# Kernel tuning notes

Measured on AMD Instinct MI355X. Metric: run time of the kernel, lower is better.

Reference implementation:

```python
import jax, jax.numpy as jnp
import numpy as np

B, S, D, H = 2, 2048, 1024, 16
HD = D // H


def setup_inputs() -> dict:
    key = jax.random.key(0)
    ks = jax.random.split(key, 16)
    sc = 0.02
    return {
        "hidden_states": jax.random.normal(ks[0], (B, S, D), jnp.float32),
        "Wq": jax.random.normal(ks[1], (D, D), jnp.float32) * sc,
        "bq": jnp.zeros((D,), jnp.float32),
        "Wk": jax.random.normal(ks[2], (D, D), jnp.float32) * sc,
        "bk": jnp.zeros((D,), jnp.float32),
        "Wv": jax.random.normal(ks[3], (D, D), jnp.float32) * sc,
        "bv": jnp.zeros((D,), jnp.float32),
        "Wo": jax.random.normal(ks[4], (D, D), jnp.float32) * sc,
        "bo": jnp.zeros((D,), jnp.float32),
        "rel_W": jax.random.normal(ks[5], (3, 2 * D), jnp.float32) * sc,
        "rel_b": jnp.zeros((3,), jnp.float32),
        "logical_bias": jax.random.normal(ks[6], (H, 3), jnp.float32) * sc,
        "gate_W": jax.random.normal(ks[7], (H, D), jnp.float32) * sc,
        "gate_b": jnp.zeros((H,), jnp.float32),
    }


def reference(hidden_states, Wq, bq, Wk, bk, Wv, bv, Wo, bo,
              rel_W, rel_b, logical_bias, gate_W, gate_b):
    x = hidden_states
    b, s, d = x.shape
    h = gate_W.shape[0]
    hd = d // h
    scale = hd ** 0.5

    q = (x @ Wq.T + bq).reshape(b, s, h, hd)
    k = (x @ Wk.T + bk).reshape(b, s, h, hd)
    v = (x @ Wv.T + bv).reshape(b, s, h, hd)

    # [b, h, i, j] raw attention scores
    attn_scores = jnp.einsum('bihd,bjhd->bhij', q, k) / scale

    # Pairwise relation logits WITHOUT materializing the [b,s,s,2d] concat:
    # cat([h_i, h_j]) @ W.T == h_i @ W[:, :d].T + h_j @ W[:, d:].T
    li = x @ rel_W[:, :d].T   # (b, s, 3) contribution from position i
    lj = x @ rel_W[:, d:].T   # (b, s, 3) contribution from position j
    logits = li[:, :, None, :] + lj[:, None, :, :] + rel_b  # (b, s, s, 3)
    relation_probs = jax.nn.softmax(logits, axis=-1)

    bias = jnp.einsum('bijk,hk->bhij', relation_probs, logical_bias)

    gate = jax.nn.sigmoid(x @ gate_W.T + gate_b)        # (b, s, h)
    gate = jnp.transpose(gate, (0, 2, 1))[..., None]    # (b, h, s, 1)

    attn_scores = attn_scores + gate * bias
    attn_weights = jax.nn.softmax(attn_scores, axis=-1)

    out = jnp.einsum('bhij,bjhd->bihd', attn_weights, v).reshape(b, s, d)
    return out @ Wo.T + bo
```

## Files before the change

### kernel.cpp

```cpp
#include <hip/hip_runtime.h>
#include <math.h>

#define B_   2
#define S_   2048
#define D_   1024
#define H_   16
#define NROW (B_ * S_)

typedef __bf16 bf16_t;
typedef __bf16 bf16x8 __attribute__((ext_vector_type(8)));
typedef __bf16 bf16x4v __attribute__((ext_vector_type(4)));
typedef float  f32x4  __attribute__((ext_vector_type(4)));

#define MFMA16(a, b, c) __builtin_amdgcn_mfma_f32_16x16x32_bf16((a), (b), (c), 0, 0, 0)

__device__ __forceinline__ void glds16(const void* src, void* lds) {
    __builtin_amdgcn_global_load_lds(
        (const __attribute__((address_space(1))) void*)src,
        (__attribute__((address_space(3))) void*)lds, 16, 0, 0);
}

__global__ __launch_bounds__(256)
void cvt_all(const float* __restrict__ x, const float* __restrict__ wq,
             const float* __restrict__ wk, const float* __restrict__ wv,
             const float* __restrict__ wo, bf16_t* __restrict__ xb,
             bf16_t* __restrict__ wqb, bf16_t* __restrict__ wkb,
             bf16_t* __restrict__ wvb, bf16_t* __restrict__ wob) {
    int bid = blockIdx.x;
    const float* src;
    bf16_t* dst;
    int base;
    if (bid < 4096) { src = x; dst = xb; base = bid; }
    else {
        int k = (bid - 4096) >> 10;
        base = (bid - 4096) & 1023;
        src = (k == 0) ? wq : (k == 1) ? wk : (k == 2) ? wv : wo;
        dst = (k == 0) ? wqb : (k == 1) ? wkb : (k == 2) ? wvb : wob;
    }
    int idx = base * 1024 + threadIdx.x * 4;
    float4 v = *(const float4*)&src[idx];
    bf16x4v o;
    o[0] = (bf16_t)v.x; o[1] = (bf16_t)v.y; o[2] = (bf16_t)v.z; o[3] = (bf16_t)v.w;
    *(bf16x4v*)&dst[idx] = o;
}

__global__ __launch_bounds__(256)
void proj_small(const float* __restrict__ x, const float* __restrict__ relW,
                const float* __restrict__ relB, const float* __restrict__ gateW,
                const float* __restrict__ gateB,
                float* __restrict__ EA4, float* __restrict__ EB4,
                float* __restrict__ GA) {
    const int wave = threadIdx.x >> 6;
    const int lane = threadIdx.x & 63;
    const int row  = blockIdx.x * 4 + wave;

    const float* xr = x + (size_t)row * D_;
    float xv[16];
    #pragma unroll
    for (int t = 0; t < 16; ++t) xv[t] = xr[lane + 64 * t];

    for (int c = 0; c < 22; ++c) {
        const float* w;
        if (c < 3)       w = relW + c * (2 * D_);
        else if (c < 6)  w = relW + (c - 3) * (2 * D_) + D_;
        else             w = gateW + (size_t)(c - 6) * D_;
        float s = 0.f;
        #pragma unroll
        for (int t = 0; t < 16; ++t) s += xv[t] * w[lane + 64 * t];
        #pragma unroll
        for (int off = 32; off; off >>= 1) s += __shfl_xor(s, off);
        if (lane == 0) {
            if (c < 3)      EA4[row * 4 + c] = expf(s + relB[c]);
            else if (c < 6) EB4[row * 4 + (c - 3)] = expf(s);
            else            GA[row * H_ + (c - 6)] =
                                1.f / (1.f + expf(-(s + gateB[c - 6])));
        }
    }
}

template<int OUTBF16>
__global__ __launch_bounds__(256)
void gemm_bf16(const bf16_t* __restrict__ A, const bf16_t* __restrict__ W,
               const float* __restrict__ bias, void* __restrict__ Cout,
               int N, int K, float scale) {
    __shared__ __align__(16) bf16_t As[128 * 32];
    __shared__ __align__(16) bf16_t Bs[128 * 32];

    const int tid = threadIdx.x, w = tid >> 6, l = tid & 63;
    const int row0 = blockIdx.y * 128, col0 = blockIdx.x * 128;
    const int wr = w >> 1, wc = w & 1;
    const int p16 = l & 15, g4 = l >> 4;

    f32x4 acc[4][4];
    #pragma unroll
    for (int i = 0; i < 4; ++i)
        #pragma unroll
        for (int j = 0; j < 4; ++j) acc[i][j] = (f32x4){0.f, 0.f, 0.f, 0.f};

    const int r0 = l >> 2, ch = l & 3;
    const int r1 = 16 + r0;
    const int ca0 = (ch ^ ((r0 >> 1) & 3)) << 3;
    const int ca1 = (ch ^ ((r1 >> 1) & 3)) << 3;
    const bf16_t* aS = A + (size_t)(row0 + w * 32) * K;
    const bf16_t* bS = W + (size_t)(col0 + w * 32) * K;
    bf16_t* aD = As + w * 1024;
    bf16_t* bD = Bs + w * 1024;

    for (int k0 = 0; k0 < K; k0 += 32) {
        glds16(aS + (size_t)r0 * K + k0 + ca0, aD);
        glds16(aS + (size_t)r1 * K + k0 + ca1, aD + 512);
        glds16(bS + (size_t)r0 * K + k0 + ca0, bD);
        glds16(bS + (size_t)r1 * K + k0 + ca1, bD + 512);
        __syncthreads();

        bf16x8 af[4], bfr[4];
        #pragma unroll
        for (int mi = 0; mi < 4; ++mi) {
            int row = wr * 64 + mi * 16 + p16;
            int chk = g4 ^ ((row >> 1) & 3);
            af[mi] = *(const bf16x8*)&As[row * 32 + chk * 8];
        }
        #pragma unroll
        for (int nj = 0; nj < 4; ++nj) {
            int row = wc * 64 + nj * 16 + p16;
            int chk = g4 ^ ((row >> 1) & 3);
            bfr[nj] = *(const bf16x8*)&Bs[row * 32 + chk * 8];
        }
        #pragma unroll
        for (int mi = 0; mi < 4; ++mi)
            #pragma unroll
            for (int nj = 0; nj < 4; ++nj)
                acc[mi][nj] = MFMA16(af[mi], bfr[nj], acc[mi][nj]);
        __syncthreads();
    }

    const int cj = col0 + wc * 64 + p16;
    #pragma unroll
    for (int nj = 0; nj < 4; ++nj) {
        int j = cj + nj * 16;
        float bj = bias[j];
        #pragma unroll
        for (int mi = 0; mi < 4; ++mi) {
            int ib = row0 + wr * 64 + mi * 16 + g4 * 4;
            #pragma unroll
            for (int r = 0; r < 4; ++r) {
                float v = (acc[mi][nj][r] + bj) * scale;
                if (OUTBF16)
                    ((bf16_t*)Cout)[(size_t)(ib + r) * N + j] = (bf16_t)v;
                else
                    ((float*)Cout)[(size_t)(ib + r) * N + j] = v;
            }
        }
    }
}

__global__ __launch_bounds__(256)
void flash_mfma(const bf16_t* __restrict__ Q, const bf16_t* __restrict__ Kg,
                const bf16_t* __restrict__ Vg, const float4* __restrict__ EA4,
                const float4* __restrict__ EB4, const float* __restrict__ GA,
                const float* __restrict__ LB, bf16_t* __restrict__ AO) {
    __shared__ __align__(16) bf16_t Ks[64 * 64];
    __shared__ __align__(16) bf16_t Vt[64 * 64];
    __shared__ __align__(16) bf16_t Ps[4][16 * 64];
    __shared__ __align__(16) float  ebs[64 * 4];

    const int tid = threadIdx.x, w = tid >> 6, l = tid & 63;
    const int b = blockIdx.y >> 4, h = blockIdx.y & 15;
    const int i0 = blockIdx.x * 64;
    const size_t rowb = (size_t)b * S_ + i0;
    const int p16 = l & 15, g4 = l >> 4;

    const float lb0 = LB[h * 3 + 0], lb1 = LB[h * 3 + 1], lb2 = LB[h * 3 + 2];

    bf16x8 qf[2];
    {
        const bf16_t* qp = Q + (rowb + w * 16 + p16) * D_ + h * 64 + g4 * 8;
        qf[0] = *(const bf16x8*)qp;
        qf[1] = *(const bf16x8*)(qp + 32);
    }

    float eaR[4][3], cnR[4][3];
    float lsum[4] = {0.f, 0.f, 0.f, 0.f};
    #pragma unroll
    for (int r = 0; r < 4; ++r) {
        size_t gi = rowb + w * 16 + g4 * 4 + r;
        float4 e = EA4[gi];
        float g = GA[gi * H_ + h];
        eaR[r][0] = e.x; eaR[r][1] = e.y; eaR[r][2] = e.z;
        cnR[r][0] = g * e.x * lb0; cnR[r][1] = g * e.y * lb1; cnR[r][2] = g * e.z * lb2;
    }

    f32x4 o[4];
    #pragma unroll
    for (int nb = 0; nb < 4; ++nb) o[nb] = (f32x4){0.f, 0.f, 0.f, 0.f};

    const int vj = tid >> 2, vc = (tid & 3) * 16;
    const int kr0 = l >> 3, kc0 = l & 7;

    for (int j0 = 0; j0 < S_; j0 += 64) {
        const size_t jb = (size_t)b * S_ + j0;
        {
            int rowA = w * 16 + kr0;
            int rowB = rowA + 8;
            glds16(Kg + (jb + rowA) * D_ + h * 64 + ((kc0 ^ (rowA & 7)) << 3),
                   Ks + w * 1024);
            glds16(Kg + (jb + rowB) * D_ + h * 64 + ((kc0 ^ (rowB & 7)) << 3),
                   Ks + w * 1024 + 512);
        }
        bf16x8 v0, v1;
        {
            const bf16_t* vp = Vg + (jb + vj) * D_ + h * 64 + vc;
            v0 = *(const bf16x8*)vp;
            v1 = *(const bf16x8*)(vp + 8);
        }
        if (tid < 64) *(float4*)&ebs[tid * 4] = EB4[jb + tid];
        #pragma unroll
        for (int u = 0; u < 8; ++u) {
            int hd = vc + u;
            int sw = ((hd & 7) ^ ((hd >> 3) & 7)) << 3;
            Vt[hd * 64 + (vj ^ sw)] = v0[u];
        }
        #pragma unroll
        for (int u = 0; u < 8; ++u) {
            int hd = vc + 8 + u;
            int sw = ((hd & 7) ^ ((hd >> 3) & 7)) << 3;
            Vt[hd * 64 + (vj ^ sw)] = v1[u];
        }
        __syncthreads();

        f32x4 s[4];
        #pragma unroll
        for (int nb = 0; nb < 4; ++nb) {
            s[nb] = (f32x4){0.f, 0.f, 0.f, 0.f};
            int row = nb * 16 + p16;
            int sw = row & 7;
            bf16x8 k0v = *(const bf16x8*)&Ks[row * 64 + ((g4    ) ^ sw) * 8];
            bf16x8 k1v = *(const bf16x8*)&Ks[row * 64 + ((g4 + 4) ^ sw) * 8];
            s[nb] = MFMA16(qf[0], k0v, s[nb]);
            s[nb] = MFMA16(qf[1], k1v, s[nb]);
        }

        #pragma unroll
        for (int nb = 0; nb < 4; ++nb) {
            float4 eb = *(const float4*)&ebs[(nb * 16 + p16) * 4];
            #pragma unroll
            for (int r = 0; r < 4; ++r) {
                float Nv = cnR[r][0] * eb.x + cnR[r][1] * eb.y + cnR[r][2] * eb.z;
                float Dv = eaR[r][0] * eb.x + eaR[r][1] * eb.y + eaR[r][2] * eb.z;
                float sv = s[nb][r] + Nv * __builtin_amdgcn_rcpf(Dv);
                float p = __expf(sv);
                bf16_t pb = (bf16_t)p;
                lsum[r] += (float)pb;
                int irow = g4 * 4 + r;
                int jcol = nb * 16 + p16;
                Ps[w][irow * 64 + (jcol ^ ((irow & 7) << 3))] = pb;
            }
        }

        bf16x8 pf0, pf1;
        {
            int sw = p16 & 7;
            pf0 = *(const bf16x8*)&Ps[w][p16 * 64 + ((g4    ) ^ sw) * 8];
            pf1 = *(const bf16x8*)&Ps[w][p16 * 64 + ((g4 + 4) ^ sw) * 8];
        }
        #pragma unroll
        for (int nb = 0; nb < 4; ++nb) {
            int vrow = nb * 16 + p16;
            int sw = (vrow & 7) ^ ((vrow >> 3) & 7);
            bf16x8 vf0 = *(const bf16x8*)&Vt[vrow * 64 + ((g4    ) ^ sw) * 8];
            bf16x8 vf1 = *(const bf16x8*)&Vt[vrow * 64 + ((g4 + 4) ^ sw) * 8];
            o[nb] = MFMA16(pf0, vf0, o[nb]);
            o[nb] = MFMA16(pf1, vf1, o[nb]);
        }
        __syncthreads();
    }

    #pragma unroll
    for (int r = 0; r < 4; ++r) {
        float t = lsum[r];
        t += __shfl_xor(t, 1); t += __shfl_xor(t, 2);
        t += __shfl_xor(t, 4); t += __shfl_xor(t, 8);
        lsum[r] = 1.f / t;
    }
    #pragma unroll
    for (int nb = 0; nb < 4; ++nb)
        #pragma unroll
        for (int r = 0; r < 4; ++r) {
            size_t gi = rowb + w * 16 + g4 * 4 + r;
            AO[gi * D_ + h * 64 + nb * 16 + p16] = (bf16_t)(o[nb][r] * lsum[r]);
        }
}

extern "C" void kernel_launch(void* const* d_in, const int* in_sizes, int n_in,
                              void* d_out, int out_size, void* d_ws, size_t ws_size,
                              hipStream_t stream) {
    const float* x    = (const float*)d_in[0];
    const float* Wq   = (const float*)d_in[1];
    const float* bq   = (const float*)d_in[2];
    const float* Wk   = (const float*)d_in[3];
    const float* bk   = (const float*)d_in[4];
    const float* Wv   = (const float*)d_in[5];
    const float* bv   = (const float*)d_in[6];
    const float* Wo   = (const float*)d_in[7];
    const float* bo   = (const float*)d_in[8];
    const float* relW = (const float*)d_in[9];
    const float* relB = (const float*)d_in[10];
    const float* lb   = (const float*)d_in[11];
    const float* gW   = (const float*)d_in[12];
    const float* gb   = (const float*)d_in[13];

    uint8_t* W8 = (uint8_t*)d_ws;
    bf16_t* xb  = (bf16_t*)(W8);
    bf16_t* wqb = (bf16_t*)(W8 + (8u  << 20));
    bf16_t* wkb = (bf16_t*)(W8 + (10u << 20));
    bf16_t* wvb = (bf16_t*)(W8 + (12u << 20));
    bf16_t* wob = (bf16_t*)(W8 + (14u << 20));
    bf16_t* Qb  = (bf16_t*)(W8 + (16u << 20));
    bf16_t* Kb  = (bf16_t*)(W8 + (24u << 20));
    bf16_t* Vb  = (bf16_t*)(W8 + (32u << 20));
    bf16_t* AOb = (bf16_t*)(W8 + (40u << 20));
    float*  EA  = (float*)(W8 + (48u << 20));
    float*  EB  = (float*)(W8 + (48u << 20) + NROW * 16);
    float*  GAp = (float*)(W8 + (48u << 20) + NROW * 32);

    cvt_all<<<8192, 256, 0, stream>>>(x, Wq, Wk, Wv, Wo, xb, wqb, wkb, wvb, wob);
    proj_small<<<NROW / 4, 256, 0, stream>>>(x, relW, relB, gW, gb, EA, EB, GAp);

    dim3 gg(D_ / 128, NROW / 128);
    gemm_bf16<1><<<gg, 256, 0, stream>>>(xb, wqb, bq, Qb, D_, D_, 0.125f);
    gemm_bf16<1><<<gg, 256, 0, stream>>>(xb, wkb, bk, Kb, D_, D_, 1.f);
    gemm_bf16<1><<<gg, 256, 0, stream>>>(xb, wvb, bv, Vb, D_, D_, 1.f);

    flash_mfma<<<dim3(S_ / 64, B_ * H_), 256, 0, stream>>>(
        Qb, Kb, Vb, (const float4*)EA, (const float4*)EB, GAp, lb, AOb);

    gemm_bf16<0><<<gg, 256, 0, stream>>>(AOb, wob, bo, d_out, D_, D_, 1.f);
}
```

Before: 335.1 us.

## Fuse QKV GEMMs, widen K tile, compute relation bias via MFMA with exp2

```diff
diff --git a/kernel.cpp b/kernel.cpp
--- a/kernel.cpp
+++ b/kernel.cpp
@@ -6,6 +6,7 @@
 #define D_   1024
 #define H_   16
 #define NROW (B_ * S_)
+#define L2E_ 1.4426950408889634f
 
 typedef __bf16 bf16_t;
 typedef __bf16 bf16x8 __attribute__((ext_vector_type(8)));
@@ -13,6 +14,12 @@
 typedef float  f32x4  __attribute__((ext_vector_type(4)));
 
 #define MFMA16(a, b, c) __builtin_amdgcn_mfma_f32_16x16x32_bf16((a), (b), (c), 0, 0, 0)
+
+#if __has_builtin(__builtin_amdgcn_exp2f)
+#define EXP2F(x) __builtin_amdgcn_exp2f(x)
+#else
+#define EXP2F(x) exp2f(x)
+#endif
 
 __device__ __forceinline__ void glds16(const void* src, void* lds) {
     __builtin_amdgcn_global_load_lds(
@@ -78,18 +85,13 @@
     }
 }
 
-template<int OUTBF16>
-__global__ __launch_bounds__(256)
-void gemm_bf16(const bf16_t* __restrict__ A, const bf16_t* __restrict__ W,
-               const float* __restrict__ bias, void* __restrict__ Cout,
-               int N, int K, float scale) {
-    __shared__ __align__(16) bf16_t As[128 * 32];
-    __shared__ __align__(16) bf16_t Bs[128 * 32];
-
+__device__ __forceinline__ void gemm_body128(
+    const bf16_t* __restrict__ A, const bf16_t* __restrict__ W,
+    const float* __restrict__ bias, float scale, int row0, int col0,
+    bf16_t* As, bf16_t* Bs, int outbf16, void* Cout, int N, int K)
+{
     const int tid = threadIdx.x, w = tid >> 6, l = tid & 63;
-    const int row0 = blockIdx.y * 128, col0 = blockIdx.x * 128;
-    const int wr = w >> 1, wc = w & 1;
-    const int p16 = l & 15, g4 = l >> 4;
+    const int wr = w >> 1, wc = w & 1, p16 = l & 15, g4 = l >> 4;
 
     f32x4 acc[4][4];
     #pragma unroll
@@ -97,40 +99,38 @@
         #pragma unroll
         for (int j = 0; j < 4; ++j) acc[i][j] = (f32x4){0.f, 0.f, 0.f, 0.f};
 
-    const int r0 = l >> 2, ch = l & 3;
-    const int r1 = 16 + r0;
-    const int ca0 = (ch ^ ((r0 >> 1) & 3)) << 3;
-    const int ca1 = (ch ^ ((r1 >> 1) & 3)) << 3;
+    const int sr = l >> 3, sc = l & 7;
     const bf16_t* aS = A + (size_t)(row0 + w * 32) * K;
     const bf16_t* bS = W + (size_t)(col0 + w * 32) * K;
-    bf16_t* aD = As + w * 1024;
-    bf16_t* bD = Bs + w * 1024;
-
-    for (int k0 = 0; k0 < K; k0 += 32) {
-        glds16(aS + (size_t)r0 * K + k0 + ca0, aD);
-        glds16(aS + (size_t)r1 * K + k0 + ca1, aD + 512);
-        glds16(bS + (size_t)r0 * K + k0 + ca0, bD);
-        glds16(bS + (size_t)r1 * K + k0 + ca1, bD + 512);
+
+    for (int k0 = 0; k0 < K; k0 += 64) {
+        #pragma unroll
+        for (int i = 0; i < 4; ++i) {
+            int r = i * 8 + sr;
+            int co = k0 + ((sc ^ sr) << 3);
+            glds16(aS + (size_t)r * K + co, As + (w * 32 + i * 8) * 64);
+            glds16(bS + (size_t)r * K + co, Bs + (w * 32 + i * 8) * 64);
+        }
         __syncthreads();
-
-        bf16x8 af[4], bfr[4];
-        #pragma unroll
-        for (int mi = 0; mi < 4; ++mi) {
-            int row = wr * 64 + mi * 16 + p16;
-            int chk = g4 ^ ((row >> 1) & 3);
-            af[mi] = *(const bf16x8*)&As[row * 32 + chk * 8];
-        }
-        #pragma unroll
-        for (int nj = 0; nj < 4; ++nj) {
-            int row = wc * 64 + nj * 16 + p16;
-            int chk = g4 ^ ((row >> 1) & 3);
-            bfr[nj] = *(const bf16x8*)&Bs[row * 32 + chk * 8];
-        }
-        #pragma unroll
-        for (int mi = 0; mi < 4; ++mi)
-            #pragma unroll
-            for (int nj = 0; nj < 4; ++nj)
-                acc[mi][nj] = MFMA16(af[mi], bfr[nj], acc[mi][nj]);
+        #pragma unroll
+        for (int c = 0; c < 2; ++c) {
+            bf16x8 af[4], bfr[4];
+            #pragma unroll
+            for (int mi = 0; mi < 4; ++mi) {
+                int row = wr * 64 + mi * 16 + p16;
+                af[mi] = *(const bf16x8*)&As[row * 64 + (((c * 4 + g4) ^ (row & 7)) << 3)];
+            }
+            #pragma unroll
+            for (int nj = 0; nj < 4; ++nj) {
+                int row = wc * 64 + nj * 16 + p16;
+                bfr[nj] = *(const bf16x8*)&Bs[row * 64 + (((c * 4 + g4) ^ (row & 7)) << 3)];
+            }
+            #pragma unroll
+            for (int mi = 0; mi < 4; ++mi)
+                #pragma unroll
+                for (int nj = 0; nj < 4; ++nj)
+                    acc[mi][nj] = MFMA16(af[mi], bfr[nj], acc[mi][nj]);
+        }
         __syncthreads();
     }
 
@@ -145,13 +145,42 @@
             #pragma unroll
             for (int r = 0; r < 4; ++r) {
                 float v = (acc[mi][nj][r] + bj) * scale;
-                if (OUTBF16)
+                if (outbf16)
                     ((bf16_t*)Cout)[(size_t)(ib + r) * N + j] = (bf16_t)v;
                 else
                     ((float*)Cout)[(size_t)(ib + r) * N + j] = v;
             }
         }
     }
+}
+
+__global__ __launch_bounds__(256)
+void gemm_qkv(const bf16_t* __restrict__ xb,
+              const bf16_t* __restrict__ wq, const bf16_t* __restrict__ wk,
+              const bf16_t* __restrict__ wv,
+              const float* __restrict__ bq, const float* __restrict__ bk,
+              const float* __restrict__ bv,
+              bf16_t* __restrict__ Qb, bf16_t* __restrict__ Kb,
+              bf16_t* __restrict__ Vb) {
+    __shared__ __align__(16) bf16_t As[128 * 64];
+    __shared__ __align__(16) bf16_t Bs[128 * 64];
+    const int seg = blockIdx.x >> 3;
+    const int col0 = (blockIdx.x & 7) * 128;
+    const int row0 = blockIdx.y * 128;
+    const bf16_t* W = (seg == 0) ? wq : (seg == 1) ? wk : wv;
+    const float* bias = (seg == 0) ? bq : (seg == 1) ? bk : bv;
+    bf16_t* C = (seg == 0) ? Qb : (seg == 1) ? Kb : Vb;
+    const float scale = (seg == 0) ? 0.125f * L2E_ : 1.0f;
+    gemm_body128(xb, W, bias, scale, row0, col0, As, Bs, 1, C, D_, D_);
+}
+
+__global__ __launch_bounds__(256)
+void gemm_out(const bf16_t* __restrict__ A, const bf16_t* __restrict__ wo,
+              const float* __restrict__ bo, float* __restrict__ out) {
+    __shared__ __align__(16) bf16_t As[128 * 64];
+    __shared__ __align__(16) bf16_t Bs[128 * 64];
+    gemm_body128(A, wo, bo, 1.0f, blockIdx.y * 128, blockIdx.x * 128,
+                 As, Bs, 0, out, D_, D_);
 }
 
 __global__ __launch_bounds__(256)
@@ -179,17 +208,25 @@
         qf[1] = *(const bf16x8*)(qp + 32);
     }
 
-    float eaR[4][3], cnR[4][3];
+    bf16x8 zer;
+    #pragma unroll
+    for (int u = 0; u < 8; ++u) zer[u] = (bf16_t)0.f;
+    bf16x8 cnf = zer, eaf = zer;
+    {
+        size_t gi = rowb + w * 16 + p16;
+        float4 e = EA4[gi];
+        float g = GA[gi * H_ + h] * L2E_;
+        if (g4 == 0) {
+            cnf[0] = (bf16_t)(g * e.x * lb0);
+            cnf[1] = (bf16_t)(g * e.y * lb1);
+            cnf[2] = (bf16_t)(g * e.z * lb2);
+            eaf[0] = (bf16_t)e.x;
+            eaf[1] = (bf16_t)e.y;
+            eaf[2] = (bf16_t)e.z;
+        }
+    }
+
     float lsum[4] = {0.f, 0.f, 0.f, 0.f};
-    #pragma unroll
-    for (int r = 0; r < 4; ++r) {
-        size_t gi = rowb + w * 16 + g4 * 4 + r;
-        float4 e = EA4[gi];
-        float g = GA[gi * H_ + h];
-        eaR[r][0] = e.x; eaR[r][1] = e.y; eaR[r][2] = e.z;
-        cnR[r][0] = g * e.x * lb0; cnR[r][1] = g * e.y * lb1; cnR[r][2] = g * e.z * lb2;
-    }
-
     f32x4 o[4];
     #pragma unroll
     for (int nb = 0; nb < 4; ++nb) o[nb] = (f32x4){0.f, 0.f, 0.f, 0.f};
@@ -228,6 +265,19 @@
         }
         __syncthreads();
 
+        f32x4 nacc[4], dacc[4];
+        #pragma unroll
+        for (int nb = 0; nb < 4; ++nb) {
+            float4 e = *(const float4*)&ebs[(nb * 16 + p16) * 4];
+            bf16x8 ebf = zer;
+            if (g4 == 0) {
+                ebf[0] = (bf16_t)e.x; ebf[1] = (bf16_t)e.y; ebf[2] = (bf16_t)e.z;
+            }
+            f32x4 z4 = (f32x4){0.f, 0.f, 0.f, 0.f};
+            nacc[nb] = MFMA16(cnf, ebf, z4);
+            dacc[nb] = MFMA16(eaf, ebf, z4);
+        }
+
         f32x4 s[4];
         #pragma unroll
         for (int nb = 0; nb < 4; ++nb) {
@@ -242,13 +292,10 @@
 
         #pragma unroll
         for (int nb = 0; nb < 4; ++nb) {
-            float4 eb = *(const float4*)&ebs[(nb * 16 + p16) * 4];
             #pragma unroll
             for (int r = 0; r < 4; ++r) {
-                float Nv = cnR[r][0] * eb.x + cnR[r][1] * eb.y + cnR[r][2] * eb.z;
-                float Dv = eaR[r][0] * eb.x + eaR[r][1] * eb.y + eaR[r][2] * eb.z;
-                float sv = s[nb][r] + Nv * __builtin_amdgcn_rcpf(Dv);
-                float p = __expf(sv);
+                float sv = s[nb][r] + nacc[nb][r] * __builtin_amdgcn_rcpf(dacc[nb][r]);
+                float p = EXP2F(sv);
                 bf16_t pb = (bf16_t)p;
                 lsum[r] += (float)pb;
                 int irow = g4 * 4 + r;
@@ -326,13 +373,11 @@
     cvt_all<<<8192, 256, 0, stream>>>(x, Wq, Wk, Wv, Wo, xb, wqb, wkb, wvb, wob);
     proj_small<<<NROW / 4, 256, 0, stream>>>(x, relW, relB, gW, gb, EA, EB, GAp);
 
-    dim3 gg(D_ / 128, NROW / 128);
-    gemm_bf16<1><<<gg, 256, 0, stream>>>(xb, wqb, bq, Qb, D_, D_, 0.125f);
-    gemm_bf16<1><<<gg, 256, 0, stream>>>(xb, wkb, bk, Kb, D_, D_, 1.f);
-    gemm_bf16<1><<<gg, 256, 0, stream>>>(xb, wvb, bv, Vb, D_, D_, 1.f);
+    gemm_qkv<<<dim3(24, 32), 256, 0, stream>>>(xb, wqb, wkb, wvb, bq, bk, bv,
+                                               Qb, Kb, Vb);
 
     flash_mfma<<<dim3(S_ / 64, B_ * H_), 256, 0, stream>>>(
         Qb, Kb, Vb, (const float4*)EA, (const float4*)EB, GAp, lb, AOb);
 
-    gemm_bf16<0><<<gg, 256, 0, stream>>>(AOb, wob, bo, d_out, D_, D_, 1.f);
-}
+    gemm_out<<<dim3(8, 32), 256, 0, stream>>>(AOb, wob, bo, (float*)d_out);
+}
```

Result: faster. 298.2 us (-11.0%).
